# Kernel optimization log

Hardware: AMD Instinct MI355X
Metric: run time of the kernel (lower is better)

Reference implementation:

```python
import jax, jax.numpy as jnp
import numpy as np

B, T, D, H = 2, 2048, 1024, 16


def setup_inputs() -> dict:
    key = jax.random.key(0)
    kx, kq, kk, kv, ko = jax.random.split(key, 5)
    s = D ** -0.5  # linear-layer init scale
    return {
        "x": jax.random.normal(kx, (B, T, D), dtype=jnp.float32),
        "Wq": jax.random.normal(kq, (D, D), dtype=jnp.float32) * s,
        "Wk": jax.random.normal(kk, (D, D), dtype=jnp.float32) * s,
        "Wv": jax.random.normal(kv, (D, D), dtype=jnp.float32) * s,
        "Wo": jax.random.normal(ko, (D, D), dtype=jnp.float32) * s,
        "quadrant_weights": jnp.array([1.0, -0.5, -0.5, 0.25], dtype=jnp.float32),
    }


def reference(x, Wq, Wk, Wv, Wo, quadrant_weights):
    Bx, Tx, Dx = x.shape
    d = Dx // H          # head dim
    h = d // 2           # quadrant (half-head) dim
    scale = h ** -0.5

    # projections -> (B, H, T, d)
    q = (x @ Wq).reshape(Bx, Tx, H, d).transpose(0, 2, 1, 3)
    k = (x @ Wk).reshape(Bx, Tx, H, d).transpose(0, 2, 1, 3)
    v = (x @ Wv).reshape(Bx, Tx, H, d).transpose(0, 2, 1, 3)

    q1, q2 = q[..., :h], q[..., h:]
    k1, k2 = k[..., :h], k[..., h:]

    w = jax.nn.softmax(quadrant_weights)
    # Fused quadrant sum: w0*q1k1^T + w1*q1k2^T + w2*q2k1^T + w3*q2k2^T
    # == q1 @ (w0*k1 + w1*k2)^T + q2 @ (w2*k1 + w3*k2)^T  (same math, fewer matmuls)
    k_eff1 = w[0] * k1 + w[1] * k2
    k_eff2 = w[2] * k1 + w[3] * k2
    attn = (jnp.einsum('bhqc,bhkc->bhqk', q1, k_eff1)
            + jnp.einsum('bhqc,bhkc->bhqk', q2, k_eff2)) * scale
    attn = jax.nn.softmax(attn, axis=-1)

    out = jnp.einsum('bhqk,bhkd->bhqd', attn, v)
    out = out.transpose(0, 2, 1, 3).reshape(Bx, Tx, Dx)
    return out @ Wo
```

## Files before the change

### kernel.cpp

```cpp
#include <hip/hip_runtime.h>

typedef unsigned short u16;
typedef unsigned int u32;
typedef __attribute__((ext_vector_type(8))) short short8;
typedef __attribute__((ext_vector_type(4))) short short4v;
typedef __attribute__((ext_vector_type(4))) float f32x4;
typedef __attribute__((ext_vector_type(16))) float f32x16;
typedef __attribute__((ext_vector_type(2))) unsigned u32x2;
typedef __attribute__((ext_vector_type(4))) unsigned u32x4;

__device__ __forceinline__ u16 f2bf(float f) {
  union { float f; unsigned u; } a; a.f = f;
  unsigned u = a.u + 0x7fffu + ((a.u >> 16) & 1u);
  return (u16)(u >> 16);
}

__device__ __forceinline__ u32 cvtpk(float lo, float hi_) {
  u32 r; asm("v_cvt_pk_bf16_f32 %0, %1, %2" : "=v"(r) : "v"(lo), "v"(hi_)); return r;
}
__device__ __forceinline__ short8 as_short8(u32x4 v) {
  union { u32x4 u; short8 s; } c; c.u = v; return c.s;
}
__device__ __forceinline__ u32 sh32(u32 v) {
  return (u32)__shfl_xor((int)v, 32, 64);
}
__device__ __forceinline__ float max3f(float a, float b, float c) {
  return fmaxf(fmaxf(a, b), c);
}

__global__ void cvt_x_kernel(const float* __restrict__ x, u16* __restrict__ xb) {
  int i = (blockIdx.x * 256 + threadIdx.x) * 8;
  float4 a = *(const float4*)(x + i);
  float4 b = *(const float4*)(x + i + 4);
  short8 v;
  v[0] = (short)f2bf(a.x); v[1] = (short)f2bf(a.y);
  v[2] = (short)f2bf(a.z); v[3] = (short)f2bf(a.w);
  v[4] = (short)f2bf(b.x); v[5] = (short)f2bf(b.y);
  v[6] = (short)f2bf(b.z); v[7] = (short)f2bf(b.w);
  *(short8*)(xb + i) = v;
}

__global__ void prep_w_kernel(const float* __restrict__ Wq, const float* __restrict__ Wk,
                              const float* __restrict__ Wv, const float* __restrict__ Wo,
                              const float* __restrict__ qw,
                              u16* __restrict__ Wcat, u16* __restrict__ Wot) {
  __shared__ float tile[32][33];
  const int z = blockIdx.z;
  const int n0 = blockIdx.x * 32, k0 = blockIdx.y * 32;
  const float* src = (z == 0) ? Wq : (z == 1) ? Wk : (z == 2) ? Wv : Wo;
  float w0 = 0.f, w1 = 0.f, w2 = 0.f, w3 = 0.f;
  if (z == 1) {
    float a = qw[0], b = qw[1], c = qw[2], d = qw[3];
    float mx = fmaxf(fmaxf(a, b), fmaxf(c, d));
    float ea = expf(a - mx), eb = expf(b - mx), ec = expf(c - mx), ed = expf(d - mx);
    float s = ea + eb + ec + ed;
    w0 = ea / s; w1 = eb / s; w2 = ec / s; w3 = ed / s;
  }
  #pragma unroll
  for (int i = 0; i < 32; i += 8) {
    int k = k0 + threadIdx.y + i;
    int n = n0 + threadIdx.x;
    float v;
    if (z == 1) {
      int c = n & 63;
      if (c < 32) v = w0 * src[k * 1024 + n]      + w1 * src[k * 1024 + n + 32];
      else        v = w2 * src[k * 1024 + n - 32] + w3 * src[k * 1024 + n];
    } else {
      v = src[k * 1024 + n];
    }
    tile[threadIdx.y + i][threadIdx.x] = v;
  }
  __syncthreads();
  #pragma unroll
  for (int i = 0; i < 32; i += 8) {
    int n = n0 + threadIdx.y + i;
    int k = k0 + threadIdx.x;
    u16 v = f2bf(tile[threadIdx.x][threadIdx.y + i]);
    if (z < 3) Wcat[(size_t)(z * 1024 + n) * 1024 + k] = v;
    else       Wot[(size_t)n * 1024 + k] = v;
  }
}

template<int MODE>
__global__ __launch_bounds__(256, 2)
void gemm_k(const u16* __restrict__ A, const u16* __restrict__ Bm,
            u16* __restrict__ out_q, u16* __restrict__ out_k,
            u16* __restrict__ out_vt, float* __restrict__ out_f) {
  __shared__ u16 At[128 * 32];
  __shared__ u16 Bt[128 * 32];
  const int tid = threadIdx.x;
  const int wid = tid >> 6, lane = tid & 63;
  const int l15 = lane & 15, l4 = lane >> 4;
  const int mblk = blockIdx.y * 128, nblk = blockIdx.x * 128;
  const int wm = (wid >> 1) * 64, wn = (wid & 1) * 64;
  f32x4 acc[4][4] = {};

  const int rA = wid * 32 + (lane >> 2);
  const int cA = (lane & 3) * 8;
  const u16* gA = A  + (size_t)(mblk + rA) * 1024 + cA;
  const u16* gB = Bm + (size_t)(nblk + rA) * 1024 + cA;

  for (int kt = 0; kt < 1024; kt += 32) {
    __syncthreads();
    #pragma unroll
    for (int q = 0; q < 2; ++q) {
      __builtin_amdgcn_global_load_lds(
          (__attribute__((address_space(1))) void*)(u16*)(gA + (size_t)q * 16 * 1024 + kt),
          (__attribute__((address_space(3))) void*)(At + (wid * 32 + q * 16) * 32),
          16, 0, 0);
      __builtin_amdgcn_global_load_lds(
          (__attribute__((address_space(1))) void*)(u16*)(gB + (size_t)q * 16 * 1024 + kt),
          (__attribute__((address_space(3))) void*)(Bt + (wid * 32 + q * 16) * 32),
          16, 0, 0);
    }
    __syncthreads();
    short8 af[4], bf[4];
    #pragma unroll
    for (int t = 0; t < 4; ++t) {
      af[t] = *(const short8*)(At + (wm + t * 16 + l15) * 32 + l4 * 8);
      bf[t] = *(const short8*)(Bt + (wn + t * 16 + l15) * 32 + l4 * 8);
    }
    #pragma unroll
    for (int i = 0; i < 4; ++i)
      #pragma unroll
      for (int j = 0; j < 4; ++j)
        acc[i][j] = __builtin_amdgcn_mfma_f32_16x16x32_bf16(af[i], bf[j], acc[i][j], 0, 0, 0);
  }

  const float QSCALE = 0.17677669529663687f * 1.4426950408889634f;
  #pragma unroll
  for (int i = 0; i < 4; ++i) {
    int m_g = mblk + wm + i * 16 + l4 * 4;
    #pragma unroll
    for (int j = 0; j < 4; ++j) {
      int n_g = nblk + wn + j * 16 + l15;
      f32x4 v = acc[i][j];
      if (MODE == 1) {
        #pragma unroll
        for (int jj = 0; jj < 4; ++jj)
          out_f[(size_t)(m_g + jj) * 1024 + n_g] = v[jj];
      } else {
        if (n_g < 2048) {
          u16* dst; float sc;
          if (n_g < 1024) { dst = out_q; sc = QSCALE; } else { dst = out_k; sc = 1.0f; }
          int nn = n_g & 1023;
          #pragma unroll
          for (int jj = 0; jj < 4; ++jj)
            dst[(size_t)(m_g + jj) * 1024 + nn] = f2bf(v[jj] * sc);
        } else {
          int c = n_g - 2048;
          int b = m_g >> 11, t = m_g & 2047;
          short4v p;
          p[0] = (short)f2bf(v[0]); p[1] = (short)f2bf(v[1]);
          p[2] = (short)f2bf(v[2]); p[3] = (short)f2bf(v[3]);
          *(short4v*)(out_vt + ((size_t)((b << 4) + (c >> 6)) * 64 + (c & 63)) * 2048 + t) = p;
        }
      }
    }
  }
}

__global__ __launch_bounds__(256)
void attn_k(const u16* __restrict__ Q, const u16* __restrict__ Kb,
            const u16* __restrict__ Vt, u16* __restrict__ O) {
  __shared__ u16 lk[2][64 * 64];
  __shared__ u16 lv[2][64 * 64];
  const int tid = threadIdx.x, wid = tid >> 6, lane = tid & 63;
  const int l31 = lane & 31, hi = lane >> 5;
  const int qt = blockIdx.x, bh = blockIdx.y;
  const int b = bh >> 4, h = bh & 15;
  const int qrow = qt * 128 + wid * 32 + l31;

  short8 qf[4];
  #pragma unroll
  for (int cs = 0; cs < 4; ++cs)
    qf[cs] = *(const short8*)(Q + (size_t)(b * 2048 + qrow) * 1024 + h * 64 + cs * 16 + hi * 8);

  const int sr = lane >> 3;
  const int sc8 = (lane & 7) ^ sr;
  const u16* Kg = Kb + (size_t)b * 2048 * 1024 + h * 64 + sc8 * 8;
  const u16* Vg = Vt + (size_t)bh * 64 * 2048 + sc8 * 8;
  const int s0i = wid * 2;

  short8 onesf;
  #pragma unroll
  for (int j = 0; j < 8; ++j) onesf[j] = (short)0x3F80;

  f32x16 accO0 = {}, accO1 = {}, sacc = {};
  float mrun = -1e30f;

  #pragma unroll
  for (int s2 = 0; s2 < 2; ++s2) {
    int s = s0i + s2;
    int r = s * 8 + sr;
    __builtin_amdgcn_global_load_lds(
      (__attribute__((address_space(1))) void*)(u16*)(Kg + (size_t)r * 1024),
      (__attribute__((address_space(3))) void*)(&lk[0][s * 512]), 16, 0, 0);
    __builtin_amdgcn_global_load_lds(
      (__attribute__((address_space(1))) void*)(u16*)(Vg + (size_t)r * 2048),
      (__attribute__((address_space(3))) void*)(&lv[0][s * 512]), 16, 0, 0);
  }
  __syncthreads();

  int cur = 0;
  const int swz = l31 & 7;

  for (int t = 0; t < 32; ++t) {
    const int kt = t * 64;
    if (t < 31) {
      #pragma unroll
      for (int s2 = 0; s2 < 2; ++s2) {
        int s = s0i + s2;
        int r = s * 8 + sr;
        __builtin_amdgcn_global_load_lds(
          (__attribute__((address_space(1))) void*)(u16*)(Kg + (size_t)(kt + 64 + r) * 1024),
          (__attribute__((address_space(3))) void*)(&lk[cur ^ 1][s * 512]), 16, 0, 0);
        __builtin_amdgcn_global_load_lds(
          (__attribute__((address_space(1))) void*)(u16*)(Vg + (size_t)r * 2048 + kt + 64),
          (__attribute__((address_space(3))) void*)(&lv[cur ^ 1][s * 512]), 16, 0, 0);
      }
    }
    const u16* kb = lk[cur];
    const u16* vb = lv[cur];

    f32x16 s0v = {}, s1v = {};
    #pragma unroll
    for (int cs = 0; cs < 4; ++cs) {
      int ch = cs * 2 + hi;
      short8 k0 = *(const short8*)(kb + l31 * 64 + ((ch ^ swz) * 8));
      short8 k1 = *(const short8*)(kb + (32 + l31) * 64 + ((ch ^ swz) * 8));
      s0v = __builtin_amdgcn_mfma_f32_32x32x16_bf16(k0, qf[cs], s0v, 0, 0, 0);
      s1v = __builtin_amdgcn_mfma_f32_32x32x16_bf16(k1, qf[cs], s1v, 0, 0, 0);
    }

    float m01 = max3f(s0v[0], s0v[1], s0v[2]);
    float m02 = max3f(s0v[3], s0v[4], s0v[5]);
    float m03 = max3f(s0v[6], s0v[7], s0v[8]);
    float m04 = max3f(s0v[9], s0v[10], s0v[11]);
    float m05 = max3f(s0v[12], s0v[13], s0v[14]);
    float m11 = max3f(s1v[0], s1v[1], s1v[2]);
    float m12 = max3f(s1v[3], s1v[4], s1v[5]);
    float m13 = max3f(s1v[6], s1v[7], s1v[8]);
    float m14 = max3f(s1v[9], s1v[10], s1v[11]);
    float m15 = max3f(s1v[12], s1v[13], s1v[14]);
    float ma = max3f(m01, m02, m03);
    float mb = max3f(m04, m05, s0v[15]);
    float mc = max3f(m11, m12, m13);
    float md = max3f(m14, m15, s1v[15]);
    float mx = fmaxf(fmaxf(ma, mb), fmaxf(mc, md));
    mx = fmaxf(mx, __shfl_xor(mx, 32, 64));

    if (!__all(mx <= mrun + 8.0f)) {
      float mnew = fmaxf(mrun, mx);
      float al = exp2f(mrun - mnew);
      mrun = mnew;
      sacc[0] *= al;
      #pragma unroll
      for (int i = 0; i < 16; ++i) { accO0[i] *= al; accO1[i] *= al; }
    }

    #pragma unroll
    for (int i = 0; i < 16; ++i) { s0v[i] = exp2f(s0v[i] - mrun); s1v[i] = exp2f(s1v[i] - mrun); }

    short8 paS[4];
    #pragma unroll
    for (int half = 0; half < 2; ++half) {
      #pragma unroll
      for (int kq = 0; kq < 2; ++kq) {
        float p0, p1, p2, p3, p4, p5, p6, p7;
        if (half == 0) {
          p0 = s0v[kq*8+0]; p1 = s0v[kq*8+1]; p2 = s0v[kq*8+2]; p3 = s0v[kq*8+3];
          p4 = s0v[kq*8+4]; p5 = s0v[kq*8+5]; p6 = s0v[kq*8+6]; p7 = s0v[kq*8+7];
        } else {
          p0 = s1v[kq*8+0]; p1 = s1v[kq*8+1]; p2 = s1v[kq*8+2]; p3 = s1v[kq*8+3];
          p4 = s1v[kq*8+4]; p5 = s1v[kq*8+5]; p6 = s1v[kq*8+6]; p7 = s1v[kq*8+7];
        }
        u32 A = cvtpk(p0, p1), B = cvtpk(p2, p3);
        u32 C = cvtpk(p4, p5), D = cvtpk(p6, p7);
        u32 e1 = sh32(hi ? A : C);
        u32 e2 = sh32(hi ? B : D);
        u32x4 w;
        w[0] = hi ? e1 : A;
        w[1] = hi ? e2 : B;
        w[2] = hi ? C : e1;
        w[3] = hi ? D : e2;
        paS[half * 2 + kq] = as_short8(w);
      }
    }

    #pragma unroll
    for (int ks = 0; ks < 4; ++ks) {
      int ch = ks * 2 + hi;
      short8 v0 = *(const short8*)(vb + l31 * 64 + ((ch ^ swz) * 8));
      short8 v1 = *(const short8*)(vb + (32 + l31) * 64 + ((ch ^ swz) * 8));
      accO0 = __builtin_amdgcn_mfma_f32_32x32x16_bf16(v0, paS[ks], accO0, 0, 0, 0);
      accO1 = __builtin_amdgcn_mfma_f32_32x32x16_bf16(v1, paS[ks], accO1, 0, 0, 0);
      sacc  = __builtin_amdgcn_mfma_f32_32x32x16_bf16(onesf, paS[ks], sacc, 0, 0, 0);
    }

    __syncthreads();
    cur ^= 1;
  }

  float inv = 1.0f / sacc[0];
  u16* Op = O + (size_t)(b * 2048 + qrow) * 1024 + h * 64;
  #pragma unroll
  for (int g = 0; g < 4; ++g) {
    u32x2 pr;
    pr[0] = cvtpk(accO0[4*g] * inv, accO0[4*g+1] * inv);
    pr[1] = cvtpk(accO0[4*g+2] * inv, accO0[4*g+3] * inv);
    *(u32x2*)(Op + 8*g + 4*hi) = pr;
    u32x2 pr2;
    pr2[0] = cvtpk(accO1[4*g] * inv, accO1[4*g+1] * inv);
    pr2[1] = cvtpk(accO1[4*g+2] * inv, accO1[4*g+3] * inv);
    *(u32x2*)(Op + 32 + 8*g + 4*hi) = pr2;
  }
}

extern "C" void kernel_launch(void* const* d_in, const int* in_sizes, int n_in,
                              void* d_out, int out_size, void* d_ws, size_t ws_size,
                              hipStream_t stream) {
  const float* x  = (const float*)d_in[0];
  const float* Wq = (const float*)d_in[1];
  const float* Wk = (const float*)d_in[2];
  const float* Wv = (const float*)d_in[3];
  const float* Wo = (const float*)d_in[4];
  const float* qw = (const float*)d_in[5];

  char* w = (char*)d_ws;
  u16* xb   = (u16*)(w);
  u16* Wcat = (u16*)(w + (8u  << 20));
  u16* Wot  = (u16*)(w + (14u << 20));
  u16* Qb   = (u16*)(w + (16u << 20));
  u16* Kb   = (u16*)(w + (24u << 20));
  u16* Vtb  = (u16*)(w + (32u << 20));
  u16* Ob   = (u16*)(w + (40u << 20));

  cvt_x_kernel<<<2048, 256, 0, stream>>>(x, xb);
  prep_w_kernel<<<dim3(32, 32, 4), dim3(32, 8), 0, stream>>>(Wq, Wk, Wv, Wo, qw, Wcat, Wot);
  gemm_k<0><<<dim3(24, 32), 256, 0, stream>>>(xb, Wcat, Qb, Kb, Vtb, nullptr);
  attn_k<<<dim3(16, 32), 256, 0, stream>>>(Qb, Kb, Vtb, Ob);
  gemm_k<1><<<dim3(8, 32), 256, 0, stream>>>(Ob, Wot, nullptr, nullptr, nullptr, (float*)d_out);
}
```

Baseline: 145.6 us.

## Double-buffer GEMM, triple-buffer attention with QK lookahead, XCD-aware block remap

The GEMM kernel now double-buffers its LDS tiles so the next k-slice is prefetched while MFMAs run, cutting one barrier per iteration. Block IDs are remapped so consecutive tiles land on the same XCD, for better L2 locality. The output projection uses 64-row tiles to launch twice as many workgroups. The attention kernel moves to a three-stage K/V LDS ring and computes the next tile's QK^T before the current softmax to overlap MFMA with VALU work, at the cost of more LDS and registers.

```diff
diff --git a/kernel.cpp b/kernel.cpp
--- a/kernel.cpp
+++ b/kernel.cpp
@@ -26,6 +26,11 @@
 }
 __device__ __forceinline__ float max3f(float a, float b, float c) {
   return fmaxf(fmaxf(a, b), c);
+}
+__device__ __forceinline__ void gload16(const u16* g, u16* l) {
+  __builtin_amdgcn_global_load_lds(
+      (__attribute__((address_space(1))) void*)(u16*)g,
+      (__attribute__((address_space(3))) void*)l, 16, 0, 0);
 }
 
 __global__ void cvt_x_kernel(const float* __restrict__ x, u16* __restrict__ xb) {
@@ -81,55 +86,71 @@
   }
 }
 
-template<int MODE>
+template<int MODE, int BM>
 __global__ __launch_bounds__(256, 2)
 void gemm_k(const u16* __restrict__ A, const u16* __restrict__ Bm,
             u16* __restrict__ out_q, u16* __restrict__ out_k,
             u16* __restrict__ out_vt, float* __restrict__ out_f) {
-  __shared__ u16 At[128 * 32];
-  __shared__ u16 Bt[128 * 32];
+  constexpr int WM = BM / 2;
+  constexpr int MR = WM / 16;
+  __shared__ u16 At[2][BM * 32];
+  __shared__ u16 Bt[2][128 * 32];
   const int tid = threadIdx.x;
   const int wid = tid >> 6, lane = tid & 63;
   const int l15 = lane & 15, l4 = lane >> 4;
-  const int mblk = blockIdx.y * 128, nblk = blockIdx.x * 128;
-  const int wm = (wid >> 1) * 64, wn = (wid & 1) * 64;
-  f32x4 acc[4][4] = {};
-
-  const int rA = wid * 32 + (lane >> 2);
+
+  const int nwg = gridDim.x * gridDim.y;
+  const int cpx = nwg >> 3;
+  int bid = blockIdx.y * gridDim.x + blockIdx.x;
+  int wg = (bid & 7) * cpx + (bid >> 3);
+  const int bx = wg % gridDim.x, by = wg / gridDim.x;
+  const int mblk = by * BM, nblk = bx * 128;
+  const int wm = (wid >> 1) * WM, wn = (wid & 1) * 64;
+  f32x4 acc[MR][4] = {};
+
+  const int rr = lane >> 2;
   const int cA = (lane & 3) * 8;
-  const u16* gA = A  + (size_t)(mblk + rA) * 1024 + cA;
-  const u16* gB = Bm + (size_t)(nblk + rA) * 1024 + cA;
-
+  const u16* gB = Bm + (size_t)(nblk + wid * 32 + rr) * 1024 + cA;
+  const u16* gA = (BM == 128) ? A + (size_t)(mblk + wid * 32 + rr) * 1024 + cA
+                              : A + (size_t)(mblk + wid * 16 + rr) * 1024 + cA;
+
+  auto STAGE = [&](int ib, int kt) {
+    if constexpr (BM == 128) {
+      #pragma unroll
+      for (int q = 0; q < 2; ++q)
+        gload16(gA + (size_t)q * 16 * 1024 + kt, &At[ib][(wid * 32 + q * 16) * 32]);
+    } else {
+      gload16(gA + kt, &At[ib][(wid * 16) * 32]);
+    }
+    #pragma unroll
+    for (int q = 0; q < 2; ++q)
+      gload16(gB + (size_t)q * 16 * 1024 + kt, &Bt[ib][(wid * 32 + q * 16) * 32]);
+  };
+
+  STAGE(0, 0);
+  __syncthreads();
+  int cur = 0;
   for (int kt = 0; kt < 1024; kt += 32) {
-    __syncthreads();
-    #pragma unroll
-    for (int q = 0; q < 2; ++q) {
-      __builtin_amdgcn_global_load_lds(
-          (__attribute__((address_space(1))) void*)(u16*)(gA + (size_t)q * 16 * 1024 + kt),
-          (__attribute__((address_space(3))) void*)(At + (wid * 32 + q * 16) * 32),
-          16, 0, 0);
-      __builtin_amdgcn_global_load_lds(
-          (__attribute__((address_space(1))) void*)(u16*)(gB + (size_t)q * 16 * 1024 + kt),
-          (__attribute__((address_space(3))) void*)(Bt + (wid * 32 + q * 16) * 32),
-          16, 0, 0);
-    }
-    __syncthreads();
-    short8 af[4], bf[4];
-    #pragma unroll
-    for (int t = 0; t < 4; ++t) {
-      af[t] = *(const short8*)(At + (wm + t * 16 + l15) * 32 + l4 * 8);
-      bf[t] = *(const short8*)(Bt + (wn + t * 16 + l15) * 32 + l4 * 8);
-    }
-    #pragma unroll
-    for (int i = 0; i < 4; ++i)
+    if (kt + 32 < 1024) STAGE(cur ^ 1, kt + 32);
+    short8 af[MR], bf[4];
+    #pragma unroll
+    for (int i = 0; i < MR; ++i)
+      af[i] = *(const short8*)(&At[cur][(wm + i * 16 + l15) * 32 + l4 * 8]);
+    #pragma unroll
+    for (int j = 0; j < 4; ++j)
+      bf[j] = *(const short8*)(&Bt[cur][(wn + j * 16 + l15) * 32 + l4 * 8]);
+    #pragma unroll
+    for (int i = 0; i < MR; ++i)
       #pragma unroll
       for (int j = 0; j < 4; ++j)
         acc[i][j] = __builtin_amdgcn_mfma_f32_16x16x32_bf16(af[i], bf[j], acc[i][j], 0, 0, 0);
+    __syncthreads();
+    cur ^= 1;
   }
 
   const float QSCALE = 0.17677669529663687f * 1.4426950408889634f;
   #pragma unroll
-  for (int i = 0; i < 4; ++i) {
+  for (int i = 0; i < MR; ++i) {
     int m_g = mblk + wm + i * 16 + l4 * 4;
     #pragma unroll
     for (int j = 0; j < 4; ++j) {
@@ -163,11 +184,14 @@
 __global__ __launch_bounds__(256)
 void attn_k(const u16* __restrict__ Q, const u16* __restrict__ Kb,
             const u16* __restrict__ Vt, u16* __restrict__ O) {
-  __shared__ u16 lk[2][64 * 64];
-  __shared__ u16 lv[2][64 * 64];
+  __shared__ u16 lk[3][64 * 64];
+  __shared__ u16 lv[3][64 * 64];
   const int tid = threadIdx.x, wid = tid >> 6, lane = tid & 63;
   const int l31 = lane & 31, hi = lane >> 5;
-  const int qt = blockIdx.x, bh = blockIdx.y;
+
+  int bid = blockIdx.y * 16 + blockIdx.x;
+  int wg = (bid & 7) * 64 + (bid >> 3);
+  const int qt = wg & 15, bh = wg >> 4;
   const int b = bh >> 4, h = bh & 15;
   const int qrow = qt * 128 + wid * 32 + l31;
 
@@ -181,6 +205,7 @@
   const u16* Kg = Kb + (size_t)b * 2048 * 1024 + h * 64 + sc8 * 8;
   const u16* Vg = Vt + (size_t)bh * 64 * 2048 + sc8 * 8;
   const int s0i = wid * 2;
+  const int swz = l31 & 7;
 
   short8 onesf;
   #pragma unroll
@@ -189,49 +214,32 @@
   f32x16 accO0 = {}, accO1 = {}, sacc = {};
   float mrun = -1e30f;
 
-  #pragma unroll
-  for (int s2 = 0; s2 < 2; ++s2) {
-    int s = s0i + s2;
-    int r = s * 8 + sr;
-    __builtin_amdgcn_global_load_lds(
-      (__attribute__((address_space(1))) void*)(u16*)(Kg + (size_t)r * 1024),
-      (__attribute__((address_space(3))) void*)(&lk[0][s * 512]), 16, 0, 0);
-    __builtin_amdgcn_global_load_lds(
-      (__attribute__((address_space(1))) void*)(u16*)(Vg + (size_t)r * 2048),
-      (__attribute__((address_space(3))) void*)(&lv[0][s * 512]), 16, 0, 0);
-  }
-  __syncthreads();
-
-  int cur = 0;
-  const int swz = l31 & 7;
-
-  for (int t = 0; t < 32; ++t) {
-    const int kt = t * 64;
-    if (t < 31) {
-      #pragma unroll
-      for (int s2 = 0; s2 < 2; ++s2) {
-        int s = s0i + s2;
-        int r = s * 8 + sr;
-        __builtin_amdgcn_global_load_lds(
-          (__attribute__((address_space(1))) void*)(u16*)(Kg + (size_t)(kt + 64 + r) * 1024),
-          (__attribute__((address_space(3))) void*)(&lk[cur ^ 1][s * 512]), 16, 0, 0);
-        __builtin_amdgcn_global_load_lds(
-          (__attribute__((address_space(1))) void*)(u16*)(Vg + (size_t)r * 2048 + kt + 64),
-          (__attribute__((address_space(3))) void*)(&lv[cur ^ 1][s * 512]), 16, 0, 0);
-      }
-    }
-    const u16* kb = lk[cur];
-    const u16* vb = lv[cur];
-
-    f32x16 s0v = {}, s1v = {};
+  auto STAGE = [&](int tt, int ib) {
+    #pragma unroll
+    for (int s2 = 0; s2 < 2; ++s2) {
+      int s = s0i + s2;
+      int r = s * 8 + sr;
+      gload16(Kg + (size_t)(tt * 64 + r) * 1024, &lk[ib][s * 512]);
+      gload16(Vg + (size_t)r * 2048 + tt * 64, &lv[ib][s * 512]);
+    }
+  };
+  auto QK = [&](int ib, f32x16& sv0, f32x16& sv1) {
+    const u16* kb = lk[ib];
+    f32x16 a0 = {}, a1 = {};
     #pragma unroll
     for (int cs = 0; cs < 4; ++cs) {
       int ch = cs * 2 + hi;
       short8 k0 = *(const short8*)(kb + l31 * 64 + ((ch ^ swz) * 8));
       short8 k1 = *(const short8*)(kb + (32 + l31) * 64 + ((ch ^ swz) * 8));
-      s0v = __builtin_amdgcn_mfma_f32_32x32x16_bf16(k0, qf[cs], s0v, 0, 0, 0);
-      s1v = __builtin_amdgcn_mfma_f32_32x32x16_bf16(k1, qf[cs], s1v, 0, 0, 0);
-    }
+      a0 = __builtin_amdgcn_mfma_f32_32x32x16_bf16(k0, qf[cs], a0, 0, 0, 0);
+      a1 = __builtin_amdgcn_mfma_f32_32x32x16_bf16(k1, qf[cs], a1, 0, 0, 0);
+    }
+    sv0 = a0; sv1 = a1;
+  };
+
+  auto BODY = [&](int t, f32x16& s0v, f32x16& s1v, f32x16& n0v, f32x16& n1v) {
+    if (t + 2 < 32) STAGE(t + 2, (t + 2) % 3);
+    if (t + 1 < 32) QK((t + 1) % 3, n0v, n1v);
 
     float m01 = max3f(s0v[0], s0v[1], s0v[2]);
     float m02 = max3f(s0v[3], s0v[4], s0v[5]);
@@ -288,6 +296,7 @@
       }
     }
 
+    const u16* vb = lv[t % 3];
     #pragma unroll
     for (int ks = 0; ks < 4; ++ks) {
       int ch = ks * 2 + hi;
@@ -299,7 +308,17 @@
     }
 
     __syncthreads();
-    cur ^= 1;
+  };
+
+  STAGE(0, 0);
+  STAGE(1, 1);
+  __syncthreads();
+  f32x16 sA0, sA1, sB0, sB1;
+  QK(0, sA0, sA1);
+
+  for (int t = 0; t < 32; t += 2) {
+    BODY(t, sA0, sA1, sB0, sB1);
+    BODY(t + 1, sB0, sB1, sA0, sA1);
   }
 
   float inv = 1.0f / sacc[0];
@@ -338,7 +357,7 @@
 
   cvt_x_kernel<<<2048, 256, 0, stream>>>(x, xb);
   prep_w_kernel<<<dim3(32, 32, 4), dim3(32, 8), 0, stream>>>(Wq, Wk, Wv, Wo, qw, Wcat, Wot);
-  gemm_k<0><<<dim3(24, 32), 256, 0, stream>>>(xb, Wcat, Qb, Kb, Vtb, nullptr);
+  gemm_k<0, 128><<<dim3(24, 32), 256, 0, stream>>>(xb, Wcat, Qb, Kb, Vtb, nullptr);
   attn_k<<<dim3(16, 32), 256, 0, stream>>>(Qb, Kb, Vtb, Ob);
-  gemm_k<1><<<dim3(8, 32), 256, 0, stream>>>(Ob, Wot, nullptr, nullptr, nullptr, (float*)d_out);
-}
+  gemm_k<1, 64><<<dim3(8, 64), 256, 0, stream>>>(Ob, Wot, nullptr, nullptr, nullptr, (float*)d_out);
+}
```

Result: slower. 181.0 us (+24.3%).
